# Optimization experiments

Measured on AMD Instinct MI355X. Metric: run time of the kernel, lower is better.

The kernel has to match this reference:

```python
import jax, jax.numpy as jnp
import numpy as np

B, S, E, FFN, Q = 8, 2048, 512, 2048, 8


def setup_inputs() -> dict:
    key = jax.random.key(0)
    k0, k1, k2, k3 = jax.random.split(key, 4)
    x = jax.random.normal(k0, (B, S, E), dtype=jnp.float32)
    ry = jax.random.normal(k1, (Q,), dtype=jnp.float32)  # trainable RY angles
    w1 = jax.random.normal(k2, (FFN, Q), dtype=jnp.float32) / np.sqrt(Q).astype(np.float32)
    b1 = jnp.zeros((FFN,), dtype=jnp.float32)
    w2 = jax.random.normal(k3, (E, FFN), dtype=jnp.float32) / np.sqrt(FFN).astype(np.float32)
    b2 = jnp.zeros((E,), dtype=jnp.float32)
    return {"x": x, "ry": ry, "w1": w1, "b1": b1, "w2": w2, "b2": b2}


def reference(x, ry, w1, b1, w2, b2):
    # Quantum layer: each qubit i starts in |0>, gets RX(x[..., i]) then RY(ry[i]),
    # then PauliZ expectation. Product state => closed form <Z_i> = cos(x_i) * cos(ry_i).
    nq = ry.shape[0]
    z = jnp.cos(x[..., :nq]) * jnp.cos(ry)  # [B, S, Q]
    # dropout is identity in eval mode
    h = jnp.einsum("bsq,fq->bsf", z, w1) + b1  # fc1
    return jnp.einsum("bsf,ef->bse", jax.nn.relu(h), w2) + b2  # fc2
```

## Files before the change

kernel.cpp:

```cpp
#include <hip/hip_runtime.h>
#include <cstdint>
#include <cstddef>


typedef __attribute__((ext_vector_type(8))) short s16x8;
typedef __attribute__((ext_vector_type(4))) float f32x4;

__device__ __forceinline__ unsigned short f2bf(float f) {
  unsigned int u = __float_as_uint(f);
  unsigned int r = u + 0x7fffu + ((u >> 16) & 1u);
  return (unsigned short)(r >> 16);
}

__device__ __forceinline__ void async_copy16(const void* g, void* l) {
  __builtin_amdgcn_global_load_lds(
      (const __attribute__((address_space(1))) void*)(uintptr_t)g,
      (__attribute__((address_space(3))) void*)(unsigned int)(uintptr_t)l,
      16, 0, 0);
}

__global__ __launch_bounds__(256) void k_w2(const float* __restrict__ w2,
                                            unsigned short* __restrict__ w2b) {
  size_t i = ((size_t)blockIdx.x * 256 + threadIdx.x) * 4;
  float4 v = *(const float4*)(w2 + i);
  uint2 p;
  p.x = f2bf(v.x) | ((unsigned)f2bf(v.y) << 16);
  p.y = f2bf(v.z) | ((unsigned)f2bf(v.w) << 16);
  *(uint2*)(w2b + i) = p;
}

__global__ __launch_bounds__(512, 2) void k_fused(
    const float* __restrict__ x, const float* __restrict__ ry,
    const float* __restrict__ w1, const float* __restrict__ b1,
    const unsigned short* __restrict__ w2b, const float* __restrict__ b2,
    float* __restrict__ C) {
  __shared__ unsigned short As[2][128 * 32];
  __shared__ unsigned short Bs[2][256 * 32];
  __shared__ float w1s[2048 * 8];
  __shared__ float b1s[2048];

  const int t = threadIdx.x;
  const int lane = t & 63;
  const int w = t >> 6;
  const int mt = (int)(blockIdx.x >> 1);
  const int nt = (int)(blockIdx.x & 1);
  const int r0 = mt * 128;
  const int c0 = nt * 256;
  const int fp = t & 15;
  const int rq = t >> 4;

  const unsigned short* gB =
      w2b + (size_t)(c0 + (t >> 2)) * 2048 + (t & 3) * 8;
  char* lB = (char*)Bs + t * 16;
  async_copy16(gB, lB);
  async_copy16(gB + (size_t)128 * 2048, lB + 8192);
#pragma unroll
  for (int i = 0; i < 8; ++i)
    async_copy16(w1 + ((size_t)t + i * 512) * 4,
                 (char*)w1s + ((size_t)t + i * 512) * 16);
  async_copy16(b1 + (size_t)t * 4, (char*)b1s + (size_t)t * 16);
  async_copy16(gB + 32, lB + 16384);
  async_copy16(gB + 32 + (size_t)128 * 2048, lB + 16384 + 8192);

  float zr[4][8];
  {
    float4 ra = *(const float4*)ry;
    float4 rb = *(const float4*)(ry + 4);
    float cy[8] = {__cosf(ra.x), __cosf(ra.y), __cosf(ra.z), __cosf(ra.w),
                   __cosf(rb.x), __cosf(rb.y), __cosf(rb.z), __cosf(rb.w)};
#pragma unroll
    for (int r = 0; r < 4; ++r) {
      const float* xr = x + (size_t)(r0 + rq * 4 + r) * 512;
      float4 x0 = *(const float4*)xr;
      float4 x1 = *(const float4*)(xr + 4);
      zr[r][0] = __cosf(x0.x) * cy[0];
      zr[r][1] = __cosf(x0.y) * cy[1];
      zr[r][2] = __cosf(x0.z) * cy[2];
      zr[r][3] = __cosf(x0.w) * cy[3];
      zr[r][4] = __cosf(x1.x) * cy[4];
      zr[r][5] = __cosf(x1.y) * cy[5];
      zr[r][6] = __cosf(x1.z) * cy[6];
      zr[r][7] = __cosf(x1.w) * cy[7];
    }
  }

  asm volatile("s_waitcnt vmcnt(0) lgkmcnt(0)" ::: "memory");
  __builtin_amdgcn_sched_barrier(0);
  __builtin_amdgcn_s_barrier();

  char* aswr = (char*)As + (size_t)rq * 4 * 64 + fp * 4;
  auto act = [&](int s, int b) {
    const float* wrow = w1s + ((size_t)s * 32 + fp * 2) * 8;
    f32x4 v0 = *(const f32x4*)(wrow);
    f32x4 v1 = *(const f32x4*)(wrow + 4);
    f32x4 v2 = *(const f32x4*)(wrow + 8);
    f32x4 v3 = *(const f32x4*)(wrow + 12);
    float b0 = b1s[s * 32 + fp * 2];
    float b1v = b1s[s * 32 + fp * 2 + 1];
    char* dst = aswr + b * 8192;
#pragma unroll
    for (int r = 0; r < 4; ++r) {
      float h0 = b0, h1 = b1v;
      h0 += zr[r][0] * v0[0]; h1 += zr[r][0] * v2[0];
      h0 += zr[r][1] * v0[1]; h1 += zr[r][1] * v2[1];
      h0 += zr[r][2] * v0[2]; h1 += zr[r][2] * v2[2];
      h0 += zr[r][3] * v0[3]; h1 += zr[r][3] * v2[3];
      h0 += zr[r][4] * v1[0]; h1 += zr[r][4] * v3[0];
      h0 += zr[r][5] * v1[1]; h1 += zr[r][5] * v3[1];
      h0 += zr[r][6] * v1[2]; h1 += zr[r][6] * v3[2];
      h0 += zr[r][7] * v1[3]; h1 += zr[r][7] * v3[3];
      h0 = fmaxf(h0, 0.0f);
      h1 = fmaxf(h1, 0.0f);
      unsigned int u;
      asm("v_cvt_pk_bf16_f32 %0, %1, %2" : "=v"(u) : "v"(h0), "v"(h1));
      *(unsigned int*)(dst + r * 64) = u;
    }
  };

  act(0, 0);

  const int wm = (w >> 2) * 64;
  const int wn = (w & 3) * 64;
  const int fr = lane & 15;
  const int quad = lane >> 4;

  f32x4 acc[4][4];
#pragma unroll
  for (int i = 0; i < 4; ++i)
#pragma unroll
    for (int j = 0; j < 4; ++j) acc[i][j] = (f32x4){0.f, 0.f, 0.f, 0.f};

  const char* pAb = (const char*)As + (size_t)(wm + fr) * 64 + quad * 16;
  const char* pBb = (const char*)Bs + (size_t)(wn + fr) * 64 + quad * 16;

  for (int kt = 0; kt < 64; ++kt) {
    const int cur = kt & 1;

    asm volatile("s_waitcnt vmcnt(2) lgkmcnt(0)" ::: "memory");
    __builtin_amdgcn_sched_barrier(0);
    __builtin_amdgcn_s_barrier();

    s16x8 af[4], bfv[4];
    const char* pA = pAb + cur * 8192;
    const char* pB = pBb + cur * 16384;
#pragma unroll
    for (int i = 0; i < 4; ++i) af[i] = *(const s16x8*)(pA + i * 1024);
#pragma unroll
    for (int j = 0; j < 4; ++j) bfv[j] = *(const s16x8*)(pB + j * 1024);

    if (kt < 63) act(kt + 1, cur ^ 1);

#pragma unroll
    for (int i = 0; i < 4; ++i)
#pragma unroll
      for (int j = 0; j < 4; ++j)
        acc[i][j] = __builtin_amdgcn_mfma_f32_16x16x32_bf16(af[i], bfv[j],
                                                            acc[i][j], 0, 0, 0);

    asm volatile("s_waitcnt lgkmcnt(0)" ::: "memory");
    __builtin_amdgcn_sched_barrier(0);
    __builtin_amdgcn_s_barrier();

    if (kt < 62) {
      const unsigned short* g = gB + (kt + 2) * 32;
      char* l = lB + cur * 16384;
      async_copy16(g, l);
      async_copy16(g + (size_t)128 * 2048, l + 8192);
    }
  }

  float bias[4];
#pragma unroll
  for (int j = 0; j < 4; ++j) bias[j] = b2[c0 + wn + j * 16 + fr];
#pragma unroll
  for (int i = 0; i < 4; ++i) {
    const int rbase = r0 + wm + i * 16 + quad * 4;
#pragma unroll
    for (int rr = 0; rr < 4; ++rr) {
      float* crow = C + (size_t)(rbase + rr) * 512;
#pragma unroll
      for (int j = 0; j < 4; ++j)
        crow[c0 + wn + j * 16 + fr] = acc[i][j][rr] + bias[j];
    }
  }
}

__global__ __launch_bounds__(256) void k_naive(
    const float* __restrict__ x, const float* __restrict__ ry,
    const float* __restrict__ w1, const float* __restrict__ b1,
    const float* __restrict__ w2, const float* __restrict__ b2,
    float* __restrict__ out) {
  __shared__ float zsh[8];
  __shared__ float acts[2048];
  const int r = blockIdx.x;
  const int t = threadIdx.x;
  if (t < 8) zsh[t] = __cosf(x[(size_t)r * 512 + t]) * __cosf(ry[t]);
  __syncthreads();
  float z[8];
#pragma unroll
  for (int q = 0; q < 8; ++q) z[q] = zsh[q];
#pragma unroll
  for (int i = 0; i < 8; ++i) {
    const int f = t * 8 + i;
    const float* wr = w1 + (size_t)f * 8;
    float4 a = *(const float4*)wr;
    float4 b = *(const float4*)(wr + 4);
    float h = b1[f] + z[0] * a.x + z[1] * a.y + z[2] * a.z + z[3] * a.w +
              z[4] * b.x + z[5] * b.y + z[6] * b.z + z[7] * b.w;
    acts[f] = fmaxf(h, 0.0f);
  }
  __syncthreads();
  for (int ee = 0; ee < 2; ++ee) {
    const int e = t + ee * 256;
    const float* wr = w2 + (size_t)e * 2048;
    float acc = b2[e];
    for (int f = 0; f < 2048; f += 4) {
      float4 wv = *(const float4*)(wr + f);
      float4 av = *(const float4*)(acts + f);
      acc += av.x * wv.x + av.y * wv.y + av.z * wv.z + av.w * wv.w;
    }
    out[(size_t)r * 512 + e] = acc;
  }
}

extern "C" void kernel_launch(void* const* d_in, const int* in_sizes, int n_in,
                              void* d_out, int out_size, void* d_ws,
                              size_t ws_size, hipStream_t stream) {
  const float* x  = (const float*)d_in[0];
  const float* ry = (const float*)d_in[1];
  const float* w1 = (const float*)d_in[2];
  const float* b1 = (const float*)d_in[3];
  const float* w2 = (const float*)d_in[4];
  const float* b2 = (const float*)d_in[5];
  float* out = (float*)d_out;

  const size_t w2b_bytes = (size_t)512 * 2048 * 2;
  if (ws_size < w2b_bytes) {
    k_naive<<<dim3(16384), dim3(256), 0, stream>>>(x, ry, w1, b1, w2, b2, out);
    return;
  }
  unsigned short* w2b = (unsigned short*)d_ws;
  k_w2<<<dim3(1024), dim3(256), 0, stream>>>(w2, w2b);
  k_fused<<<dim3(256), dim3(512), 0, stream>>>(x, ry, w1, b1, w2b, b2, out);
}
```

Baseline: 151.3 us.

## Pre-tile W2 into an LDS-friendly image and swizzle A/w1 shared layouts

Result: faster. 148.3 us (-2.0%).

```diff
diff --git a/kernel.cpp b/kernel.cpp
--- a/kernel.cpp
+++ b/kernel.cpp
@@ -20,13 +20,21 @@
 }
 
 __global__ __launch_bounds__(256) void k_w2(const float* __restrict__ w2,
-                                            unsigned short* __restrict__ w2b) {
-  size_t i = ((size_t)blockIdx.x * 256 + threadIdx.x) * 4;
-  float4 v = *(const float4*)(w2 + i);
-  uint2 p;
-  p.x = f2bf(v.x) | ((unsigned)f2bf(v.y) << 16);
-  p.y = f2bf(v.z) | ((unsigned)f2bf(v.w) << 16);
-  *(uint2*)(w2b + i) = p;
+                                            unsigned short* __restrict__ img) {
+  const int n = blockIdx.x;
+  const int t = threadIdx.x;
+  const int s = t >> 2, quad = t & 3;
+  const float* src = w2 + (size_t)n * 2048 + t * 8;
+  float4 a = *(const float4*)src;
+  float4 b = *(const float4*)(src + 4);
+  uint4 pk;
+  pk.x = f2bf(a.x) | ((unsigned)f2bf(a.y) << 16);
+  pk.y = f2bf(a.z) | ((unsigned)f2bf(a.w) << 16);
+  pk.z = f2bf(b.x) | ((unsigned)f2bf(b.y) << 16);
+  pk.w = f2bf(b.z) | ((unsigned)f2bf(b.w) << 16);
+  const int nt = n >> 8, nl = n & 255, nhi = nl >> 4, nlo = nl & 15;
+  const size_t ci = (size_t)(nt * 64 + s) * 1024 + nhi * 64 + quad * 16 + nlo;
+  *(uint4*)(img + ci * 8) = pk;
 }
 
 __global__ __launch_bounds__(512, 2) void k_fused(
@@ -49,18 +57,21 @@
   const int fp = t & 15;
   const int rq = t >> 4;
 
-  const unsigned short* gB =
-      w2b + (size_t)(c0 + (t >> 2)) * 2048 + (t & 3) * 8;
+  const unsigned short* gB = w2b + (size_t)nt * 64 * 8192 + t * 8;
   char* lB = (char*)Bs + t * 16;
   async_copy16(gB, lB);
-  async_copy16(gB + (size_t)128 * 2048, lB + 8192);
-#pragma unroll
-  for (int i = 0; i < 8; ++i)
-    async_copy16(w1 + ((size_t)t + i * 512) * 4,
-                 (char*)w1s + ((size_t)t + i * 512) * 16);
+  async_copy16(gB + 4096, lB + 8192);
+#pragma unroll
+  for (int i = 0; i < 8; ++i) {
+    const int l = t + i * 512;
+    const int sl = l >> 6, wsl = l & 63;
+    const int idx = ((wsl & 15) << 2) | (wsl >> 4);
+    async_copy16(w1 + (size_t)(sl * 32 + (idx >> 1)) * 8 + (idx & 1) * 4,
+                 (char*)w1s + (size_t)l * 16);
+  }
   async_copy16(b1 + (size_t)t * 4, (char*)b1s + (size_t)t * 16);
-  async_copy16(gB + 32, lB + 16384);
-  async_copy16(gB + 32 + (size_t)128 * 2048, lB + 16384 + 8192);
+  async_copy16(gB + 8192, lB + 16384);
+  async_copy16(gB + 8192 + 4096, lB + 16384 + 8192);
 
   float zr[4][8];
   {
@@ -88,13 +99,15 @@
   __builtin_amdgcn_sched_barrier(0);
   __builtin_amdgcn_s_barrier();
 
-  char* aswr = (char*)As + (size_t)rq * 4 * 64 + fp * 4;
+  char* aswr = (char*)As + (rq >> 2) * 1024 +
+               (((((fp >> 3) & 1) << 3) | ((rq & 3) << 1) | ((fp >> 2) & 1)) << 4) +
+               (fp & 3) * 4;
   auto act = [&](int s, int b) {
-    const float* wrow = w1s + ((size_t)s * 32 + fp * 2) * 8;
-    f32x4 v0 = *(const f32x4*)(wrow);
-    f32x4 v1 = *(const f32x4*)(wrow + 4);
-    f32x4 v2 = *(const f32x4*)(wrow + 8);
-    f32x4 v3 = *(const f32x4*)(wrow + 12);
+    const char* wb = (const char*)w1s + s * 1024 + fp * 16;
+    f32x4 v0 = *(const f32x4*)(wb);
+    f32x4 v1 = *(const f32x4*)(wb + 256);
+    f32x4 v2 = *(const f32x4*)(wb + 512);
+    f32x4 v3 = *(const f32x4*)(wb + 768);
     float b0 = b1s[s * 32 + fp * 2];
     float b1v = b1s[s * 32 + fp * 2 + 1];
     char* dst = aswr + b * 8192;
@@ -113,7 +126,7 @@
       h1 = fmaxf(h1, 0.0f);
       unsigned int u;
       asm("v_cvt_pk_bf16_f32 %0, %1, %2" : "=v"(u) : "v"(h0), "v"(h1));
-      *(unsigned int*)(dst + r * 64) = u;
+      *(unsigned int*)(dst + r * 256) = u;
     }
   };
 
@@ -130,8 +143,10 @@
 #pragma unroll
     for (int j = 0; j < 4; ++j) acc[i][j] = (f32x4){0.f, 0.f, 0.f, 0.f};
 
-  const char* pAb = (const char*)As + (size_t)(wm + fr) * 64 + quad * 16;
-  const char* pBb = (const char*)Bs + (size_t)(wn + fr) * 64 + quad * 16;
+  const int slotA = ((fr & 3) << 4) | (((quad >> 1) & 1) << 3) |
+                    ((fr >> 2) << 1) | (quad & 1);
+  const char* pAb = (const char*)As + ((wm >> 4) * 1024) + slotA * 16;
+  const char* pBb = (const char*)Bs + ((wn >> 4) * 1024) + quad * 256 + fr * 16;
 
   for (int kt = 0; kt < 64; ++kt) {
     const int cur = kt & 1;
@@ -150,22 +165,24 @@
 
     if (kt < 63) act(kt + 1, cur ^ 1);
 
+    __builtin_amdgcn_s_setprio(1);
 #pragma unroll
     for (int i = 0; i < 4; ++i)
 #pragma unroll
       for (int j = 0; j < 4; ++j)
         acc[i][j] = __builtin_amdgcn_mfma_f32_16x16x32_bf16(af[i], bfv[j],
                                                             acc[i][j], 0, 0, 0);
+    __builtin_amdgcn_s_setprio(0);
 
     asm volatile("s_waitcnt lgkmcnt(0)" ::: "memory");
     __builtin_amdgcn_sched_barrier(0);
     __builtin_amdgcn_s_barrier();
 
     if (kt < 62) {
-      const unsigned short* g = gB + (kt + 2) * 32;
+      const unsigned short* g = gB + (size_t)(kt + 2) * 8192;
       char* l = lB + cur * 16384;
       async_copy16(g, l);
-      async_copy16(g + (size_t)128 * 2048, l + 8192);
+      async_copy16(g + 4096, l + 8192);
     }
   }
 
@@ -240,6 +257,6 @@
     return;
   }
   unsigned short* w2b = (unsigned short*)d_ws;
-  k_w2<<<dim3(1024), dim3(256), 0, stream>>>(w2, w2b);
+  k_w2<<<dim3(512), dim3(256), 0, stream>>>(w2, w2b);
   k_fused<<<dim3(256), dim3(512), 0, stream>>>(x, ry, w1, b1, w2b, b2, out);
 }
```
